# Optimization experiments

Hardware: AMD Instinct MI355X
Metric: run time of the kernel (lower is better)

## Reference

```python
import jax, jax.numpy as jnp
import numpy as np

N_TOK = 2048      # flattened batch*seq tokens
D_MODEL = 1024    # in_features
D_INT = 512       # d_intermediate
N_EXPERTS = 8     # n_routed_experts
TOP_K = 2         # n_activated_experts


def setup_inputs() -> dict:
    key = jax.random.key(0)
    k1, k2, k3, k4, k5 = jax.random.split(key, 5)
    x = jax.random.normal(k1, (N_TOK, D_MODEL), dtype=jnp.float32)
    indices = jax.random.randint(k2, (N_TOK, TOP_K), 0, N_EXPERTS, dtype=jnp.int32)
    # router combine weights (normalized over top-k like a softmax router)
    weights = jax.nn.softmax(jax.random.normal(k3, (N_TOK, TOP_K), dtype=jnp.float32), axis=-1)
    # tokens-per-expert counts, consistent with indices (as the router would supply)
    counts = jnp.bincount(indices.reshape(-1), length=N_EXPERTS).astype(jnp.int32)
    # expert weights: fc1 -> 2*d_int (gated MLP), fc2 -> d_model; kaiming-ish scale
    s1 = 1.0 / np.sqrt(D_MODEL)
    s2 = 1.0 / np.sqrt(D_INT)
    fc1_weight = jax.random.uniform(k4, (N_EXPERTS, 2 * D_INT, D_MODEL), jnp.float32, -s1, s1)
    fc2_weight = jax.random.uniform(k5, (N_EXPERTS, D_MODEL, D_INT), jnp.float32, -s2, s2)
    return {"x": x, "weights": weights, "indices": indices, "counts": counts,
            "fc1_weight": fc1_weight, "fc2_weight": fc2_weight}


def reference(x, weights, indices, counts, fc1_weight, fc2_weight):
    # Dense dispatch-free formulation: run every token through every expert's
    # gated MLP, then gather the per-slot expert output. Identical math to the
    # sort / grouped-GEMM / scatter path for the selected (token, expert) pairs.
    # h: (n_tok, n_experts, 2*d_int)
    h = jnp.einsum('td,egd->teg', x, fc1_weight)
    y, z = jnp.split(h, 2, axis=-1)
    a = y * jax.nn.silu(z)  # GatedMLP: y * activation(z)
    # expert outputs: (n_tok, n_experts, d_model)
    out = jnp.einsum('tei,edi->ted', a, fc2_weight)
    # gather the chosen expert output for each of the top-k slots: (n_tok, k, d_model)
    per_slot = jnp.take_along_axis(out, indices[:, :, None], axis=1)
    # combine: z = bmm(weights[:, None], x_by_expert).squeeze(1)
    return jnp.einsum('tk,tkd->td', weights, per_slot)
```

## Files before the change

### kernel.cpp

```cpp
#include <hip/hip_runtime.h>

typedef unsigned short u16;
typedef unsigned int u32;
using short8  = __attribute__((ext_vector_type(8))) short;
using floatx4 = __attribute__((ext_vector_type(4))) float;

#define N_TOK   2048
#define D_MODEL 1024
#define D_INT   512
#define NE      8

#define O_TOK    0
#define O_WROW   24576
#define O_XG     65536
#define O_ACT    10551296
#define O_FC1B   36765696
#define O_FC2B   53542912

static __device__ inline u16 f2bf(float f) {
    u32 u = __builtin_bit_cast(u32, f);
    u = (u + 0x7fffu + ((u >> 16) & 1u)) >> 16;
    return (u16)u;
}
static __device__ inline u32 pack2(float a, float b) {
    return (u32)f2bf(a) | ((u32)f2bf(b) << 16);
}
static __device__ inline void glds16(const u16* g, u16* l) {
    __builtin_amdgcn_global_load_lds(
        (const __attribute__((address_space(1))) void*)g,
        (__attribute__((address_space(3))) void*)l, 16, 0, 0);
}

__global__ __launch_bounds__(256) void prep_kernel(
    const float* __restrict__ x, const float* __restrict__ wts,
    const int* __restrict__ indices, const int* __restrict__ counts,
    const float* __restrict__ fc1, const float* __restrict__ fc2,
    u16* __restrict__ fc1b, u16* __restrict__ fc2b,
    u16* __restrict__ Xg, int* __restrict__ tok, float* __restrict__ wrow,
    float* __restrict__ out) {
    int b = blockIdx.x, tid = threadIdx.x;
    if (b < 6144) {
        size_t v = (size_t)b * 256 + tid;
        const float* src; u16* dst; size_t off;
        if (v < 1048576) { src = fc1; dst = fc1b; off = v * 8; }
        else             { src = fc2; dst = fc2b; off = (v - 1048576) * 8; }
        const floatx4* s4 = reinterpret_cast<const floatx4*>(src + off);
        floatx4 a = s4[0], bb = s4[1];
        uint4 o;
        o.x = pack2(a[0], a[1]); o.y = pack2(a[2], a[3]);
        o.z = pack2(bb[0], bb[1]); o.w = pack2(bb[2], bb[3]);
        *reinterpret_cast<uint4*>(dst + off) = o;
        return;
    }
    if (b < 8192) {
        int t = b - 6144;
        int off[NE];
        {
            int acc = 0;
            #pragma unroll
            for (int e = 0; e < NE; e++) { off[e] = acc; acc += ((counts[e] + 63) >> 6) << 6; }
        }
        int e0 = indices[2 * t], e1 = indices[2 * t + 1];
        __shared__ int s0, s1;
        if (tid == 0) { s0 = 0; s1 = 0; }
        __syncthreads();
        int c0 = 0, c1 = 0;
        const int4* ip = reinterpret_cast<const int4*>(indices);
        #pragma unroll
        for (int i = 0; i < 4; i++) {
            int4 vv = ip[tid * 4 + i];
            int q = tid * 16 + i * 4;
            c0 += (q + 0 < 2 * t && vv.x == e0) + (q + 1 < 2 * t && vv.y == e0)
                + (q + 2 < 2 * t && vv.z == e0) + (q + 3 < 2 * t && vv.w == e0);
            c1 += (q + 0 <= 2 * t && vv.x == e1) + (q + 1 <= 2 * t && vv.y == e1)
                + (q + 2 <= 2 * t && vv.z == e1) + (q + 3 <= 2 * t && vv.w == e1);
        }
        if (c0) atomicAdd(&s0, c0);
        if (c1) atomicAdd(&s1, c1);
        __syncthreads();
        int r0 = off[e0] + s0;
        int r1 = off[e1] + s1;
        if (tid == 0) {
            tok[r0] = t; tok[r1] = t;
            wrow[r0] = wts[2 * t]; wrow[r1] = wts[2 * t + 1];
        }
        const floatx4* src = reinterpret_cast<const floatx4*>(x + (size_t)t * D_MODEL);
        floatx4 a = src[tid];
        uint2 o;
        o.x = pack2(a[0], a[1]); o.y = pack2(a[2], a[3]);
        *reinterpret_cast<uint2*>(Xg + (size_t)r0 * D_MODEL + tid * 4) = o;
        *reinterpret_cast<uint2*>(Xg + (size_t)r1 * D_MODEL + tid * 4) = o;
        return;
    }
    {
        int z = b - 8192;
        floatx4* dst = reinterpret_cast<floatx4*>(out) + (size_t)z * 1024;
        #pragma unroll
        for (int i = 0; i < 4; i++) dst[i * 256 + tid] = (floatx4){0.f, 0.f, 0.f, 0.f};
        return;
    }
}

__global__ __launch_bounds__(256) void gemm1_kernel(
    const u16* __restrict__ Xg, const u16* __restrict__ fc1b,
    u16* __restrict__ Act, const int* __restrict__ counts) {
    __shared__ u16 As[64 * 64];
    __shared__ u16 Bs[128 * 64];
    int tid = threadIdx.x;
    int soff[NE + 1];
    {
        int acc = 0;
        #pragma unroll
        for (int e2 = 0; e2 < NE; e2++) { soff[e2] = acc; acc += ((counts[e2] + 63) >> 6) << 6; }
        soff[NE] = acc;
    }
    int row0 = blockIdx.y * 64;
    if (row0 >= soff[NE]) return;
    int e = 0;
    while (soff[e + 1] <= row0) e++;
    int bx = blockIdx.x;
    const u16* A  = Xg + (size_t)row0 * 1024;
    const u16* Be = fc1b + (size_t)e * 1024 * 1024;

    int lane = tid & 63, w = tid >> 6;
    int m0 = (w >> 1) * 32, n0 = (w & 1) * 32;
    int lr = lane & 15, kq = lane >> 4;

    const u16* gA[2]; u16* lA[2];
    #pragma unroll
    for (int j = 0; j < 2; j++) {
        int v = tid + j * 256;
        int r = v >> 3, kb = (v & 7) ^ (r & 7);
        gA[j] = A + (size_t)r * 1024 + kb * 8;
        lA[j] = As + (w * 64 + j * 256) * 8;
    }
    const u16* gB[4]; u16* lB[4];
    #pragma unroll
    for (int j = 0; j < 4; j++) {
        int v = tid + j * 256;
        int r = v >> 3, kb = (v & 7) ^ (r & 7);
        int grow = (r < 64) ? (bx * 64 + r) : (448 + bx * 64 + r);
        gB[j] = Be + (size_t)grow * 1024 + kb * 8;
        lB[j] = Bs + (w * 64 + j * 256) * 8;
    }

    floatx4 aY[2][2], aZ[2][2];
    #pragma unroll
    for (int i = 0; i < 2; i++)
        #pragma unroll
        for (int j = 0; j < 2; j++) {
            aY[i][j] = (floatx4){0.f, 0.f, 0.f, 0.f};
            aZ[i][j] = (floatx4){0.f, 0.f, 0.f, 0.f};
        }

    for (int k0 = 0; k0 < 1024; k0 += 64) {
        glds16(gA[0] + k0, lA[0]); glds16(gA[1] + k0, lA[1]);
        glds16(gB[0] + k0, lB[0]); glds16(gB[1] + k0, lB[1]);
        glds16(gB[2] + k0, lB[2]); glds16(gB[3] + k0, lB[3]);
        __syncthreads();
        #pragma unroll
        for (int ks = 0; ks < 2; ks++) {
            int sw = ((ks * 4 + kq) ^ (lr & 7)) * 8;
            short8 af[2], by[2], bz[2];
            #pragma unroll
            for (int i = 0; i < 2; i++)
                af[i] = *reinterpret_cast<const short8*>(&As[(m0 + i * 16 + lr) * 64 + sw]);
            #pragma unroll
            for (int j = 0; j < 2; j++) {
                by[j] = *reinterpret_cast<const short8*>(&Bs[(n0 + j * 16 + lr) * 64 + sw]);
                bz[j] = *reinterpret_cast<const short8*>(&Bs[(64 + n0 + j * 16 + lr) * 64 + sw]);
            }
            #pragma unroll
            for (int i = 0; i < 2; i++)
                #pragma unroll
                for (int j = 0; j < 2; j++) {
                    aY[i][j] = __builtin_amdgcn_mfma_f32_16x16x32_bf16(af[i], by[j], aY[i][j], 0, 0, 0);
                    aZ[i][j] = __builtin_amdgcn_mfma_f32_16x16x32_bf16(af[i], bz[j], aZ[i][j], 0, 0, 0);
                }
        }
        __syncthreads();
    }
    #pragma unroll
    for (int i = 0; i < 2; i++)
        #pragma unroll
        for (int j = 0; j < 2; j++) {
            floatx4 y = aY[i][j], z = aZ[i][j];
            #pragma unroll
            for (int r = 0; r < 4; r++) {
                float zz = z[r];
                float av = y[r] * (zz / (1.0f + __expf(-zz)));
                int m = m0 + i * 16 + kq * 4 + r;
                int g = bx * 64 + n0 + j * 16 + lr;
                Act[(size_t)(row0 + m) * D_INT + g] = f2bf(av);
            }
        }
}

__global__ __launch_bounds__(256) void gemm2_kernel(
    const u16* __restrict__ Act, const u16* __restrict__ fc2b,
    float* __restrict__ out, const int* __restrict__ counts,
    const int* __restrict__ tok, const float* __restrict__ wrow) {
    __shared__ u16 As[64 * 64];
    __shared__ u16 Bs[128 * 64];
    __shared__ int sTok[64];
    __shared__ float sW[64];
    int tid = threadIdx.x;
    int soff[NE + 1];
    {
        int acc = 0;
        #pragma unroll
        for (int e2 = 0; e2 < NE; e2++) { soff[e2] = acc; acc += ((counts[e2] + 63) >> 6) << 6; }
        soff[NE] = acc;
    }
    int row0 = blockIdx.y * 64;
    if (row0 >= soff[NE]) return;
    int e = 0;
    while (soff[e + 1] <= row0) e++;
    int bx = blockIdx.x;
    const u16* A  = Act + (size_t)row0 * 512;
    const u16* Be = fc2b + (size_t)e * 1024 * 512;

    int lane = tid & 63, w = tid >> 6;
    int m0 = (w >> 1) * 32, n0 = (w & 1) * 64;
    int lr = lane & 15, kq = lane >> 4;

    const u16* gA[2]; u16* lA[2];
    #pragma unroll
    for (int j = 0; j < 2; j++) {
        int v = tid + j * 256;
        int r = v >> 3, kb = (v & 7) ^ (r & 7);
        gA[j] = A + (size_t)r * 512 + kb * 8;
        lA[j] = As + (w * 64 + j * 256) * 8;
    }
    const u16* gB[4]; u16* lB[4];
    #pragma unroll
    for (int j = 0; j < 4; j++) {
        int v = tid + j * 256;
        int r = v >> 3, kb = (v & 7) ^ (r & 7);
        gB[j] = Be + (size_t)(bx * 128 + r) * 512 + kb * 8;
        lB[j] = Bs + (w * 64 + j * 256) * 8;
    }

    floatx4 acc[2][4];
    #pragma unroll
    for (int i = 0; i < 2; i++)
        #pragma unroll
        for (int j = 0; j < 4; j++) acc[i][j] = (floatx4){0.f, 0.f, 0.f, 0.f};

    for (int k0 = 0; k0 < 512; k0 += 64) {
        glds16(gA[0] + k0, lA[0]); glds16(gA[1] + k0, lA[1]);
        glds16(gB[0] + k0, lB[0]); glds16(gB[1] + k0, lB[1]);
        glds16(gB[2] + k0, lB[2]); glds16(gB[3] + k0, lB[3]);
        __syncthreads();
        #pragma unroll
        for (int ks = 0; ks < 2; ks++) {
            int sw = ((ks * 4 + kq) ^ (lr & 7)) * 8;
            short8 af[2], bf[4];
            #pragma unroll
            for (int i = 0; i < 2; i++)
                af[i] = *reinterpret_cast<const short8*>(&As[(m0 + i * 16 + lr) * 64 + sw]);
            #pragma unroll
            for (int j = 0; j < 4; j++)
                bf[j] = *reinterpret_cast<const short8*>(&Bs[(n0 + j * 16 + lr) * 64 + sw]);
            #pragma unroll
            for (int i = 0; i < 2; i++)
                #pragma unroll
                for (int j = 0; j < 4; j++)
                    acc[i][j] = __builtin_amdgcn_mfma_f32_16x16x32_bf16(af[i], bf[j], acc[i][j], 0, 0, 0);
        }
        __syncthreads();
    }
    if (tid < 64) {
        int g = row0 + tid;
        bool val = (g - soff[e]) < counts[e];
        sTok[tid] = val ? tok[g] : -1;
        sW[tid]   = val ? wrow[g] : 0.f;
    }
    __syncthreads();
    #pragma unroll
    for (int i = 0; i < 2; i++)
        #pragma unroll
        for (int r = 0; r < 4; r++) {
            int m = m0 + i * 16 + kq * 4 + r;
            int t = sTok[m];
            if (t >= 0) {
                float wgt = sW[m];
                float* dst = out + (size_t)t * D_MODEL + bx * 128;
                #pragma unroll
                for (int j = 0; j < 4; j++)
                    atomicAdd(dst + n0 + j * 16 + lr, wgt * acc[i][j][r]);
            }
        }
}

extern "C" void kernel_launch(void* const* d_in, const int* in_sizes, int n_in,
                              void* d_out, int out_size, void* d_ws, size_t ws_size,
                              hipStream_t stream) {
    const float* x       = (const float*)d_in[0];
    const float* wts     = (const float*)d_in[1];
    const int*   indices = (const int*)d_in[2];
    const int*   counts  = (const int*)d_in[3];
    const float* fc1     = (const float*)d_in[4];
    const float* fc2     = (const float*)d_in[5];
    float* out = (float*)d_out;
    char* ws = (char*)d_ws;

    int*   tok  = (int*)(ws + O_TOK);
    float* wrow = (float*)(ws + O_WROW);
    u16*   Xg   = (u16*)(ws + O_XG);
    u16*   Act  = (u16*)(ws + O_ACT);
    u16*   fc1b = (u16*)(ws + O_FC1B);
    u16*   fc2b = (u16*)(ws + O_FC2B);

    prep_kernel<<<8704, 256, 0, stream>>>(x, wts, indices, counts, fc1, fc2,
                                          fc1b, fc2b, Xg, tok, wrow, out);
    gemm1_kernel<<<dim3(8, 72), 256, 0, stream>>>(Xg, fc1b, Act, counts);
    gemm2_kernel<<<dim3(8, 72), 256, 0, stream>>>(Act, fc2b, out, counts, tok, wrow);
}
```

Measured before the change: 151.0 us.

## Double-buffer LDS tiles in both expert GEMMs to overlap loads with MFMA

Both grouped GEMM kernels now keep two LDS buffers. The next K-tile's global-to-LDS copies are issued before the MFMA work on the current tile, and an explicit vmcnt wait plus barriers stand in for the old per-iteration syncthreads. This is meant to hide global memory latency behind compute. In exchange, LDS use per block doubles, which may reduce occupancy, and correctness depends on the hand-written vmcnt counts matching the number of outstanding loads.

```diff
diff --git a/kernel.cpp b/kernel.cpp
--- a/kernel.cpp
+++ b/kernel.cpp
@@ -104,8 +104,8 @@
 __global__ __launch_bounds__(256) void gemm1_kernel(
     const u16* __restrict__ Xg, const u16* __restrict__ fc1b,
     u16* __restrict__ Act, const int* __restrict__ counts) {
-    __shared__ u16 As[64 * 64];
-    __shared__ u16 Bs[128 * 64];
+    __shared__ u16 As[2][64 * 64];
+    __shared__ u16 Bs[2][128 * 64];
     int tid = threadIdx.x;
     int soff[NE + 1];
     {
@@ -126,22 +126,22 @@
     int m0 = (w >> 1) * 32, n0 = (w & 1) * 32;
     int lr = lane & 15, kq = lane >> 4;
 
-    const u16* gA[2]; u16* lA[2];
+    const u16* gA[2]; int oA[2];
     #pragma unroll
     for (int j = 0; j < 2; j++) {
         int v = tid + j * 256;
         int r = v >> 3, kb = (v & 7) ^ (r & 7);
         gA[j] = A + (size_t)r * 1024 + kb * 8;
-        lA[j] = As + (w * 64 + j * 256) * 8;
-    }
-    const u16* gB[4]; u16* lB[4];
+        oA[j] = (w * 64 + j * 256) * 8;
+    }
+    const u16* gB[4]; int oB[4];
     #pragma unroll
     for (int j = 0; j < 4; j++) {
         int v = tid + j * 256;
         int r = v >> 3, kb = (v & 7) ^ (r & 7);
         int grow = (r < 64) ? (bx * 64 + r) : (448 + bx * 64 + r);
         gB[j] = Be + (size_t)grow * 1024 + kb * 8;
-        lB[j] = Bs + (w * 64 + j * 256) * 8;
+        oB[j] = (w * 64 + j * 256) * 8;
     }
 
     floatx4 aY[2][2], aZ[2][2];
@@ -153,22 +153,26 @@
             aZ[i][j] = (floatx4){0.f, 0.f, 0.f, 0.f};
         }
 
-    for (int k0 = 0; k0 < 1024; k0 += 64) {
-        glds16(gA[0] + k0, lA[0]); glds16(gA[1] + k0, lA[1]);
-        glds16(gB[0] + k0, lB[0]); glds16(gB[1] + k0, lB[1]);
-        glds16(gB[2] + k0, lB[2]); glds16(gB[3] + k0, lB[3]);
-        __syncthreads();
+    auto stage = [&](int bufi, int k0) {
+        glds16(gA[0] + k0, &As[bufi][oA[0]]);
+        glds16(gA[1] + k0, &As[bufi][oA[1]]);
+        glds16(gB[0] + k0, &Bs[bufi][oB[0]]);
+        glds16(gB[1] + k0, &Bs[bufi][oB[1]]);
+        glds16(gB[2] + k0, &Bs[bufi][oB[2]]);
+        glds16(gB[3] + k0, &Bs[bufi][oB[3]]);
+    };
+    auto compute = [&](int bufi) {
         #pragma unroll
         for (int ks = 0; ks < 2; ks++) {
             int sw = ((ks * 4 + kq) ^ (lr & 7)) * 8;
             short8 af[2], by[2], bz[2];
             #pragma unroll
             for (int i = 0; i < 2; i++)
-                af[i] = *reinterpret_cast<const short8*>(&As[(m0 + i * 16 + lr) * 64 + sw]);
+                af[i] = *reinterpret_cast<const short8*>(&As[bufi][(m0 + i * 16 + lr) * 64 + sw]);
             #pragma unroll
             for (int j = 0; j < 2; j++) {
-                by[j] = *reinterpret_cast<const short8*>(&Bs[(n0 + j * 16 + lr) * 64 + sw]);
-                bz[j] = *reinterpret_cast<const short8*>(&Bs[(64 + n0 + j * 16 + lr) * 64 + sw]);
+                by[j] = *reinterpret_cast<const short8*>(&Bs[bufi][(n0 + j * 16 + lr) * 64 + sw]);
+                bz[j] = *reinterpret_cast<const short8*>(&Bs[bufi][(64 + n0 + j * 16 + lr) * 64 + sw]);
             }
             #pragma unroll
             for (int i = 0; i < 2; i++)
@@ -178,8 +182,24 @@
                     aZ[i][j] = __builtin_amdgcn_mfma_f32_16x16x32_bf16(af[i], bz[j], aZ[i][j], 0, 0, 0);
                 }
         }
-        __syncthreads();
-    }
+    };
+
+    stage(0, 0);
+    int bufi = 0;
+    for (int k0 = 0; k0 < 960; k0 += 64) {
+        stage(bufi ^ 1, k0 + 64);
+        asm volatile("s_waitcnt vmcnt(6)" ::: "memory");
+        __builtin_amdgcn_s_barrier();
+        __builtin_amdgcn_sched_barrier(0);
+        compute(bufi);
+        __builtin_amdgcn_sched_barrier(0);
+        __builtin_amdgcn_s_barrier();
+        bufi ^= 1;
+    }
+    asm volatile("s_waitcnt vmcnt(0)" ::: "memory");
+    __builtin_amdgcn_s_barrier();
+    compute(bufi);
+
     #pragma unroll
     for (int i = 0; i < 2; i++)
         #pragma unroll
@@ -200,8 +220,8 @@
     const u16* __restrict__ Act, const u16* __restrict__ fc2b,
     float* __restrict__ out, const int* __restrict__ counts,
     const int* __restrict__ tok, const float* __restrict__ wrow) {
-    __shared__ u16 As[64 * 64];
-    __shared__ u16 Bs[128 * 64];
+    __shared__ u16 As[2][64 * 64];
+    __shared__ u16 Bs[2][128 * 64];
     __shared__ int sTok[64];
     __shared__ float sW[64];
     int tid = threadIdx.x;
@@ -224,58 +244,79 @@
     int m0 = (w >> 1) * 32, n0 = (w & 1) * 64;
     int lr = lane & 15, kq = lane >> 4;
 
-    const u16* gA[2]; u16* lA[2];
+    const u16* gA[2]; int oA[2];
     #pragma unroll
     for (int j = 0; j < 2; j++) {
         int v = tid + j * 256;
         int r = v >> 3, kb = (v & 7) ^ (r & 7);
         gA[j] = A + (size_t)r * 512 + kb * 8;
-        lA[j] = As + (w * 64 + j * 256) * 8;
-    }
-    const u16* gB[4]; u16* lB[4];
+        oA[j] = (w * 64 + j * 256) * 8;
+    }
+    const u16* gB[4]; int oB[4];
     #pragma unroll
     for (int j = 0; j < 4; j++) {
         int v = tid + j * 256;
         int r = v >> 3, kb = (v & 7) ^ (r & 7);
         gB[j] = Be + (size_t)(bx * 128 + r) * 512 + kb * 8;
-        lB[j] = Bs + (w * 64 + j * 256) * 8;
-    }
-
-    floatx4 acc[2][4];
-    #pragma unroll
-    for (int i = 0; i < 2; i++)
-        #pragma unroll
-        for (int j = 0; j < 4; j++) acc[i][j] = (floatx4){0.f, 0.f, 0.f, 0.f};
-
-    for (int k0 = 0; k0 < 512; k0 += 64) {
-        glds16(gA[0] + k0, lA[0]); glds16(gA[1] + k0, lA[1]);
-        glds16(gB[0] + k0, lB[0]); glds16(gB[1] + k0, lB[1]);
-        glds16(gB[2] + k0, lB[2]); glds16(gB[3] + k0, lB[3]);
-        __syncthreads();
-        #pragma unroll
-        for (int ks = 0; ks < 2; ks++) {
-            int sw = ((ks * 4 + kq) ^ (lr & 7)) * 8;
-            short8 af[2], bf[4];
-            #pragma unroll
-            for (int i = 0; i < 2; i++)
-                af[i] = *reinterpret_cast<const short8*>(&As[(m0 + i * 16 + lr) * 64 + sw]);
-            #pragma unroll
-            for (int j = 0; j < 4; j++)
-                bf[j] = *reinterpret_cast<const short8*>(&Bs[(n0 + j * 16 + lr) * 64 + sw]);
-            #pragma unroll
-            for (int i = 0; i < 2; i++)
-                #pragma unroll
-                for (int j = 0; j < 4; j++)
-                    acc[i][j] = __builtin_amdgcn_mfma_f32_16x16x32_bf16(af[i], bf[j], acc[i][j], 0, 0, 0);
-        }
-        __syncthreads();
-    }
+        oB[j] = (w * 64 + j * 256) * 8;
+    }
+
     if (tid < 64) {
         int g = row0 + tid;
         bool val = (g - soff[e]) < counts[e];
         sTok[tid] = val ? tok[g] : -1;
         sW[tid]   = val ? wrow[g] : 0.f;
     }
+
+    floatx4 acc[2][4];
+    #pragma unroll
+    for (int i = 0; i < 2; i++)
+        #pragma unroll
+        for (int j = 0; j < 4; j++) acc[i][j] = (floatx4){0.f, 0.f, 0.f, 0.f};
+
+    auto stage = [&](int bufi, int k0) {
+        glds16(gA[0] + k0, &As[bufi][oA[0]]);
+        glds16(gA[1] + k0, &As[bufi][oA[1]]);
+        glds16(gB[0] + k0, &Bs[bufi][oB[0]]);
+        glds16(gB[1] + k0, &Bs[bufi][oB[1]]);
+        glds16(gB[2] + k0, &Bs[bufi][oB[2]]);
+        glds16(gB[3] + k0, &Bs[bufi][oB[3]]);
+    };
+    auto compute = [&](int bufi) {
+        #pragma unroll
+        for (int ks = 0; ks < 2; ks++) {
+            int sw = ((ks * 4 + kq) ^ (lr & 7)) * 8;
+            short8 af[2], bfr[4];
+            #pragma unroll
+            for (int i = 0; i < 2; i++)
+                af[i] = *reinterpret_cast<const short8*>(&As[bufi][(m0 + i * 16 + lr) * 64 + sw]);
+            #pragma unroll
+            for (int j = 0; j < 4; j++)
+                bfr[j] = *reinterpret_cast<const short8*>(&Bs[bufi][(n0 + j * 16 + lr) * 64 + sw]);
+            #pragma unroll
+            for (int i = 0; i < 2; i++)
+                #pragma unroll
+                for (int j = 0; j < 4; j++)
+                    acc[i][j] = __builtin_amdgcn_mfma_f32_16x16x32_bf16(af[i], bfr[j], acc[i][j], 0, 0, 0);
+        }
+    };
+
+    stage(0, 0);
+    int bufi = 0;
+    for (int k0 = 0; k0 < 448; k0 += 64) {
+        stage(bufi ^ 1, k0 + 64);
+        asm volatile("s_waitcnt vmcnt(6)" ::: "memory");
+        __builtin_amdgcn_s_barrier();
+        __builtin_amdgcn_sched_barrier(0);
+        compute(bufi);
+        __builtin_amdgcn_sched_barrier(0);
+        __builtin_amdgcn_s_barrier();
+        bufi ^= 1;
+    }
+    asm volatile("s_waitcnt vmcnt(0)" ::: "memory");
+    __builtin_amdgcn_s_barrier();
+    compute(bufi);
+
     __syncthreads();
     #pragma unroll
     for (int i = 0; i < 2; i++)
```

Measured after the change: 152.1 us. About the same (+0.7%).

## Fuse fp32-to-bf16 weight conversion into GEMM B-tile loads with double buffering

Applied to the files above, without the earlier changes.

Removes the separate pass that converts all expert weights to bf16 in a workspace. The GEMMs now load fp32 weights directly into registers and convert them while writing the LDS tile, using double-buffered LDS so the next tile's loads overlap the current tile's MFMA work. Output zeroing moves into extra gemm1 blocks, and prep shrinks to token dispatch only. This drops a full write and re-read of the bf16 weights, but each GEMM block now reads twice the weight bytes from global memory and uses more LDS and registers.

```diff
diff --git a/kernel.cpp b/kernel.cpp
--- a/kernel.cpp
+++ b/kernel.cpp
@@ -14,8 +14,6 @@
 #define O_WROW   24576
 #define O_XG     65536
 #define O_ACT    10551296
-#define O_FC1B   36765696
-#define O_FC2B   53542912
 
 static __device__ inline u16 f2bf(float f) {
     u32 u = __builtin_bit_cast(u32, f);
@@ -34,79 +32,62 @@
 __global__ __launch_bounds__(256) void prep_kernel(
     const float* __restrict__ x, const float* __restrict__ wts,
     const int* __restrict__ indices, const int* __restrict__ counts,
-    const float* __restrict__ fc1, const float* __restrict__ fc2,
-    u16* __restrict__ fc1b, u16* __restrict__ fc2b,
-    u16* __restrict__ Xg, int* __restrict__ tok, float* __restrict__ wrow,
+    u16* __restrict__ Xg, int* __restrict__ tok, float* __restrict__ wrow) {
+    int t = blockIdx.x, tid = threadIdx.x;
+    int off[NE];
+    {
+        int acc = 0;
+        #pragma unroll
+        for (int e = 0; e < NE; e++) { off[e] = acc; acc += ((counts[e] + 63) >> 6) << 6; }
+    }
+    int e0 = indices[2 * t], e1 = indices[2 * t + 1];
+    __shared__ int s0, s1;
+    if (tid == 0) { s0 = 0; s1 = 0; }
+    __syncthreads();
+    int c0 = 0, c1 = 0;
+    const int4* ip = reinterpret_cast<const int4*>(indices);
+    #pragma unroll
+    for (int i = 0; i < 4; i++) {
+        int4 vv = ip[tid * 4 + i];
+        int q = tid * 16 + i * 4;
+        c0 += (q + 0 < 2 * t && vv.x == e0) + (q + 1 < 2 * t && vv.y == e0)
+            + (q + 2 < 2 * t && vv.z == e0) + (q + 3 < 2 * t && vv.w == e0);
+        c1 += (q + 0 <= 2 * t && vv.x == e1) + (q + 1 <= 2 * t && vv.y == e1)
+            + (q + 2 <= 2 * t && vv.z == e1) + (q + 3 <= 2 * t && vv.w == e1);
+    }
+    if (c0) atomicAdd(&s0, c0);
+    if (c1) atomicAdd(&s1, c1);
+    __syncthreads();
+    int r0 = off[e0] + s0;
+    int r1 = off[e1] + s1;
+    if (tid == 0) {
+        tok[r0] = t; tok[r1] = t;
+        wrow[r0] = wts[2 * t]; wrow[r1] = wts[2 * t + 1];
+    }
+    const floatx4* src = reinterpret_cast<const floatx4*>(x + (size_t)t * D_MODEL);
+    floatx4 a = src[tid];
+    uint2 o;
+    o.x = pack2(a[0], a[1]); o.y = pack2(a[2], a[3]);
+    *reinterpret_cast<uint2*>(Xg + (size_t)r0 * D_MODEL + tid * 4) = o;
+    *reinterpret_cast<uint2*>(Xg + (size_t)r1 * D_MODEL + tid * 4) = o;
+}
+
+__global__ __launch_bounds__(256) void gemm1_kernel(
+    const u16* __restrict__ Xg, const float* __restrict__ fc1,
+    u16* __restrict__ Act, const int* __restrict__ counts,
     float* __restrict__ out) {
-    int b = blockIdx.x, tid = threadIdx.x;
-    if (b < 6144) {
-        size_t v = (size_t)b * 256 + tid;
-        const float* src; u16* dst; size_t off;
-        if (v < 1048576) { src = fc1; dst = fc1b; off = v * 8; }
-        else             { src = fc2; dst = fc2b; off = (v - 1048576) * 8; }
-        const floatx4* s4 = reinterpret_cast<const floatx4*>(src + off);
-        floatx4 a = s4[0], bb = s4[1];
-        uint4 o;
-        o.x = pack2(a[0], a[1]); o.y = pack2(a[2], a[3]);
-        o.z = pack2(bb[0], bb[1]); o.w = pack2(bb[2], bb[3]);
-        *reinterpret_cast<uint4*>(dst + off) = o;
-        return;
-    }
-    if (b < 8192) {
-        int t = b - 6144;
-        int off[NE];
-        {
-            int acc = 0;
-            #pragma unroll
-            for (int e = 0; e < NE; e++) { off[e] = acc; acc += ((counts[e] + 63) >> 6) << 6; }
-        }
-        int e0 = indices[2 * t], e1 = indices[2 * t + 1];
-        __shared__ int s0, s1;
-        if (tid == 0) { s0 = 0; s1 = 0; }
-        __syncthreads();
-        int c0 = 0, c1 = 0;
-        const int4* ip = reinterpret_cast<const int4*>(indices);
-        #pragma unroll
-        for (int i = 0; i < 4; i++) {
-            int4 vv = ip[tid * 4 + i];
-            int q = tid * 16 + i * 4;
-            c0 += (q + 0 < 2 * t && vv.x == e0) + (q + 1 < 2 * t && vv.y == e0)
-                + (q + 2 < 2 * t && vv.z == e0) + (q + 3 < 2 * t && vv.w == e0);
-            c1 += (q + 0 <= 2 * t && vv.x == e1) + (q + 1 <= 2 * t && vv.y == e1)
-                + (q + 2 <= 2 * t && vv.z == e1) + (q + 3 <= 2 * t && vv.w == e1);
-        }
-        if (c0) atomicAdd(&s0, c0);
-        if (c1) atomicAdd(&s1, c1);
-        __syncthreads();
-        int r0 = off[e0] + s0;
-        int r1 = off[e1] + s1;
-        if (tid == 0) {
-            tok[r0] = t; tok[r1] = t;
-            wrow[r0] = wts[2 * t]; wrow[r1] = wts[2 * t + 1];
-        }
-        const floatx4* src = reinterpret_cast<const floatx4*>(x + (size_t)t * D_MODEL);
-        floatx4 a = src[tid];
-        uint2 o;
-        o.x = pack2(a[0], a[1]); o.y = pack2(a[2], a[3]);
-        *reinterpret_cast<uint2*>(Xg + (size_t)r0 * D_MODEL + tid * 4) = o;
-        *reinterpret_cast<uint2*>(Xg + (size_t)r1 * D_MODEL + tid * 4) = o;
-        return;
-    }
-    {
-        int z = b - 8192;
+    __shared__ u16 As[2][64 * 64];
+    __shared__ u16 Bs[2][128 * 64];
+    int tid = threadIdx.x;
+    int b = blockIdx.x;
+    if (b >= 576) {
+        int z = b - 576;
         floatx4* dst = reinterpret_cast<floatx4*>(out) + (size_t)z * 1024;
         #pragma unroll
         for (int i = 0; i < 4; i++) dst[i * 256 + tid] = (floatx4){0.f, 0.f, 0.f, 0.f};
         return;
     }
-}
-
-__global__ __launch_bounds__(256) void gemm1_kernel(
-    const u16* __restrict__ Xg, const u16* __restrict__ fc1b,
-    u16* __restrict__ Act, const int* __restrict__ counts) {
-    __shared__ u16 As[64 * 64];
-    __shared__ u16 Bs[128 * 64];
-    int tid = threadIdx.x;
+    int bx = b & 7, by = b >> 3;
     int soff[NE + 1];
     {
         int acc = 0;
@@ -114,34 +95,33 @@
         for (int e2 = 0; e2 < NE; e2++) { soff[e2] = acc; acc += ((counts[e2] + 63) >> 6) << 6; }
         soff[NE] = acc;
     }
-    int row0 = blockIdx.y * 64;
+    int row0 = by * 64;
     if (row0 >= soff[NE]) return;
     int e = 0;
     while (soff[e + 1] <= row0) e++;
-    int bx = blockIdx.x;
-    const u16* A  = Xg + (size_t)row0 * 1024;
-    const u16* Be = fc1b + (size_t)e * 1024 * 1024;
+    const u16*   A  = Xg + (size_t)row0 * 1024;
+    const float* Be = fc1 + (size_t)e * 1024 * 1024;
 
     int lane = tid & 63, w = tid >> 6;
     int m0 = (w >> 1) * 32, n0 = (w & 1) * 32;
     int lr = lane & 15, kq = lane >> 4;
 
-    const u16* gA[2]; u16* lA[2];
+    const u16* gA[2]; int oA[2];
     #pragma unroll
     for (int j = 0; j < 2; j++) {
         int v = tid + j * 256;
         int r = v >> 3, kb = (v & 7) ^ (r & 7);
         gA[j] = A + (size_t)r * 1024 + kb * 8;
-        lA[j] = As + (w * 64 + j * 256) * 8;
-    }
-    const u16* gB[4]; u16* lB[4];
+        oA[j] = (w * 64 + j * 256) * 8;
+    }
+    const float* gB[4]; int oBw[4];
     #pragma unroll
     for (int j = 0; j < 4; j++) {
         int v = tid + j * 256;
         int r = v >> 3, kb = (v & 7) ^ (r & 7);
         int grow = (r < 64) ? (bx * 64 + r) : (448 + bx * 64 + r);
         gB[j] = Be + (size_t)grow * 1024 + kb * 8;
-        lB[j] = Bs + (w * 64 + j * 256) * 8;
+        oBw[j] = v * 8;
     }
 
     floatx4 aY[2][2], aZ[2][2];
@@ -153,33 +133,69 @@
             aZ[i][j] = (floatx4){0.f, 0.f, 0.f, 0.f};
         }
 
-    for (int k0 = 0; k0 < 1024; k0 += 64) {
-        glds16(gA[0] + k0, lA[0]); glds16(gA[1] + k0, lA[1]);
-        glds16(gB[0] + k0, lB[0]); glds16(gB[1] + k0, lB[1]);
-        glds16(gB[2] + k0, lB[2]); glds16(gB[3] + k0, lB[3]);
-        __syncthreads();
+    auto computeT = [&](int bufi) {
         #pragma unroll
         for (int ks = 0; ks < 2; ks++) {
             int sw = ((ks * 4 + kq) ^ (lr & 7)) * 8;
-            short8 af[2], by[2], bz[2];
+            short8 af[2], byf[2], bzf[2];
             #pragma unroll
             for (int i = 0; i < 2; i++)
-                af[i] = *reinterpret_cast<const short8*>(&As[(m0 + i * 16 + lr) * 64 + sw]);
+                af[i] = *reinterpret_cast<const short8*>(&As[bufi][(m0 + i * 16 + lr) * 64 + sw]);
             #pragma unroll
             for (int j = 0; j < 2; j++) {
-                by[j] = *reinterpret_cast<const short8*>(&Bs[(n0 + j * 16 + lr) * 64 + sw]);
-                bz[j] = *reinterpret_cast<const short8*>(&Bs[(64 + n0 + j * 16 + lr) * 64 + sw]);
+                byf[j] = *reinterpret_cast<const short8*>(&Bs[bufi][(n0 + j * 16 + lr) * 64 + sw]);
+                bzf[j] = *reinterpret_cast<const short8*>(&Bs[bufi][(64 + n0 + j * 16 + lr) * 64 + sw]);
             }
             #pragma unroll
             for (int i = 0; i < 2; i++)
                 #pragma unroll
                 for (int j = 0; j < 2; j++) {
-                    aY[i][j] = __builtin_amdgcn_mfma_f32_16x16x32_bf16(af[i], by[j], aY[i][j], 0, 0, 0);
-                    aZ[i][j] = __builtin_amdgcn_mfma_f32_16x16x32_bf16(af[i], bz[j], aZ[i][j], 0, 0, 0);
+                    aY[i][j] = __builtin_amdgcn_mfma_f32_16x16x32_bf16(af[i], byf[j], aY[i][j], 0, 0, 0);
+                    aZ[i][j] = __builtin_amdgcn_mfma_f32_16x16x32_bf16(af[i], bzf[j], aZ[i][j], 0, 0, 0);
                 }
         }
+    };
+    auto stageB_write = [&](int bufi, const floatx4* lo, const floatx4* hi) {
+        #pragma unroll
+        for (int j = 0; j < 4; j++) {
+            uint4 o;
+            o.x = pack2(lo[j][0], lo[j][1]); o.y = pack2(lo[j][2], lo[j][3]);
+            o.z = pack2(hi[j][0], hi[j][1]); o.w = pack2(hi[j][2], hi[j][3]);
+            *reinterpret_cast<uint4*>(&Bs[bufi][oBw[j]]) = o;
+        }
+    };
+
+    {
+        floatx4 lo[4], hi[4];
+        #pragma unroll
+        for (int j = 0; j < 4; j++) {
+            lo[j] = *reinterpret_cast<const floatx4*>(gB[j]);
+            hi[j] = *reinterpret_cast<const floatx4*>(gB[j] + 4);
+        }
+        glds16(gA[0], &As[0][oA[0]]);
+        glds16(gA[1], &As[0][oA[1]]);
+        stageB_write(0, lo, hi);
         __syncthreads();
     }
+    int bufi = 0;
+    for (int k0 = 0; k0 < 1024; k0 += 64) {
+        int nk = k0 + 64;
+        floatx4 lo[4], hi[4];
+        if (nk < 1024) {
+            #pragma unroll
+            for (int j = 0; j < 4; j++) {
+                lo[j] = *reinterpret_cast<const floatx4*>(gB[j] + nk);
+                hi[j] = *reinterpret_cast<const floatx4*>(gB[j] + nk + 4);
+            }
+            glds16(gA[0] + nk, &As[bufi ^ 1][oA[0]]);
+            glds16(gA[1] + nk, &As[bufi ^ 1][oA[1]]);
+        }
+        computeT(bufi);
+        if (nk < 1024) stageB_write(bufi ^ 1, lo, hi);
+        __syncthreads();
+        bufi ^= 1;
+    }
+
     #pragma unroll
     for (int i = 0; i < 2; i++)
         #pragma unroll
@@ -197,14 +213,16 @@
 }
 
 __global__ __launch_bounds__(256) void gemm2_kernel(
-    const u16* __restrict__ Act, const u16* __restrict__ fc2b,
+    const u16* __restrict__ Act, const float* __restrict__ fc2,
     float* __restrict__ out, const int* __restrict__ counts,
     const int* __restrict__ tok, const float* __restrict__ wrow) {
-    __shared__ u16 As[64 * 64];
-    __shared__ u16 Bs[128 * 64];
+    __shared__ u16 As[2][64 * 64];
+    __shared__ u16 Bs[2][128 * 64];
     __shared__ int sTok[64];
     __shared__ float sW[64];
     int tid = threadIdx.x;
+    int b = blockIdx.x;
+    int bx = b & 7, by = b >> 3;
     int soff[NE + 1];
     {
         int acc = 0;
@@ -212,71 +230,106 @@
         for (int e2 = 0; e2 < NE; e2++) { soff[e2] = acc; acc += ((counts[e2] + 63) >> 6) << 6; }
         soff[NE] = acc;
     }
-    int row0 = blockIdx.y * 64;
+    int row0 = by * 64;
     if (row0 >= soff[NE]) return;
     int e = 0;
     while (soff[e + 1] <= row0) e++;
-    int bx = blockIdx.x;
-    const u16* A  = Act + (size_t)row0 * 512;
-    const u16* Be = fc2b + (size_t)e * 1024 * 512;
+    const u16*   A  = Act + (size_t)row0 * 512;
+    const float* Be = fc2 + (size_t)e * 1024 * 512;
 
     int lane = tid & 63, w = tid >> 6;
     int m0 = (w >> 1) * 32, n0 = (w & 1) * 64;
     int lr = lane & 15, kq = lane >> 4;
 
-    const u16* gA[2]; u16* lA[2];
+    const u16* gA[2]; int oA[2];
     #pragma unroll
     for (int j = 0; j < 2; j++) {
         int v = tid + j * 256;
         int r = v >> 3, kb = (v & 7) ^ (r & 7);
         gA[j] = A + (size_t)r * 512 + kb * 8;
-        lA[j] = As + (w * 64 + j * 256) * 8;
-    }
-    const u16* gB[4]; u16* lB[4];
+        oA[j] = (w * 64 + j * 256) * 8;
+    }
+    const float* gB[4]; int oBw[4];
     #pragma unroll
     for (int j = 0; j < 4; j++) {
         int v = tid + j * 256;
         int r = v >> 3, kb = (v & 7) ^ (r & 7);
         gB[j] = Be + (size_t)(bx * 128 + r) * 512 + kb * 8;
-        lB[j] = Bs + (w * 64 + j * 256) * 8;
-    }
-
-    floatx4 acc[2][4];
-    #pragma unroll
-    for (int i = 0; i < 2; i++)
-        #pragma unroll
-        for (int j = 0; j < 4; j++) acc[i][j] = (floatx4){0.f, 0.f, 0.f, 0.f};
-
-    for (int k0 = 0; k0 < 512; k0 += 64) {
-        glds16(gA[0] + k0, lA[0]); glds16(gA[1] + k0, lA[1]);
-        glds16(gB[0] + k0, lB[0]); glds16(gB[1] + k0, lB[1]);
-        glds16(gB[2] + k0, lB[2]); glds16(gB[3] + k0, lB[3]);
-        __syncthreads();
-        #pragma unroll
-        for (int ks = 0; ks < 2; ks++) {
-            int sw = ((ks * 4 + kq) ^ (lr & 7)) * 8;
-            short8 af[2], bf[4];
-            #pragma unroll
-            for (int i = 0; i < 2; i++)
-                af[i] = *reinterpret_cast<const short8*>(&As[(m0 + i * 16 + lr) * 64 + sw]);
-            #pragma unroll
-            for (int j = 0; j < 4; j++)
-                bf[j] = *reinterpret_cast<const short8*>(&Bs[(n0 + j * 16 + lr) * 64 + sw]);
-            #pragma unroll
-            for (int i = 0; i < 2; i++)
-                #pragma unroll
-                for (int j = 0; j < 4; j++)
-                    acc[i][j] = __builtin_amdgcn_mfma_f32_16x16x32_bf16(af[i], bf[j], acc[i][j], 0, 0, 0);
-        }
-        __syncthreads();
-    }
+        oBw[j] = v * 8;
+    }
+
     if (tid < 64) {
         int g = row0 + tid;
         bool val = (g - soff[e]) < counts[e];
         sTok[tid] = val ? tok[g] : -1;
         sW[tid]   = val ? wrow[g] : 0.f;
     }
-    __syncthreads();
+
+    floatx4 acc[2][4];
+    #pragma unroll
+    for (int i = 0; i < 2; i++)
+        #pragma unroll
+        for (int j = 0; j < 4; j++) acc[i][j] = (floatx4){0.f, 0.f, 0.f, 0.f};
+
+    auto computeT = [&](int bufi) {
+        #pragma unroll
+        for (int ks = 0; ks < 2; ks++) {
+            int sw = ((ks * 4 + kq) ^ (lr & 7)) * 8;
+            short8 af[2], bfr[4];
+            #pragma unroll
+            for (int i = 0; i < 2; i++)
+                af[i] = *reinterpret_cast<const short8*>(&As[bufi][(m0 + i * 16 + lr) * 64 + sw]);
+            #pragma unroll
+            for (int j = 0; j < 4; j++)
+                bfr[j] = *reinterpret_cast<const short8*>(&Bs[bufi][(n0 + j * 16 + lr) * 64 + sw]);
+            #pragma unroll
+            for (int i = 0; i < 2; i++)
+                #pragma unroll
+                for (int j = 0; j < 4; j++)
+                    acc[i][j] = __builtin_amdgcn_mfma_f32_16x16x32_bf16(af[i], bfr[j], acc[i][j], 0, 0, 0);
+        }
+    };
+    auto stageB_write = [&](int bufi, const floatx4* lo, const floatx4* hi) {
+        #pragma unroll
+        for (int j = 0; j < 4; j++) {
+            uint4 o;
+            o.x = pack2(lo[j][0], lo[j][1]); o.y = pack2(lo[j][2], lo[j][3]);
+            o.z = pack2(hi[j][0], hi[j][1]); o.w = pack2(hi[j][2], hi[j][3]);
+            *reinterpret_cast<uint4*>(&Bs[bufi][oBw[j]]) = o;
+        }
+    };
+
+    {
+        floatx4 lo[4], hi[4];
+        #pragma unroll
+        for (int j = 0; j < 4; j++) {
+            lo[j] = *reinterpret_cast<const floatx4*>(gB[j]);
+            hi[j] = *reinterpret_cast<const floatx4*>(gB[j] + 4);
+        }
+        glds16(gA[0], &As[0][oA[0]]);
+        glds16(gA[1], &As[0][oA[1]]);
+        stageB_write(0, lo, hi);
+        __syncthreads();
+    }
+    int bufi = 0;
+    for (int k0 = 0; k0 < 512; k0 += 64) {
+        int nk = k0 + 64;
+        floatx4 lo[4], hi[4];
+        if (nk < 512) {
+            #pragma unroll
+            for (int j = 0; j < 4; j++) {
+                lo[j] = *reinterpret_cast<const floatx4*>(gB[j] + nk);
+                hi[j] = *reinterpret_cast<const floatx4*>(gB[j] + nk + 4);
+            }
+            glds16(gA[0] + nk, &As[bufi ^ 1][oA[0]]);
+            glds16(gA[1] + nk, &As[bufi ^ 1][oA[1]]);
+        }
+        computeT(bufi);
+        if (nk < 512) stageB_write(bufi ^ 1, lo, hi);
+        __syncthreads();
+        bufi ^= 1;
+    }
+
     #pragma unroll
     for (int i = 0; i < 2; i++)
         #pragma unroll
@@ -309,11 +362,8 @@
     float* wrow = (float*)(ws + O_WROW);
     u16*   Xg   = (u16*)(ws + O_XG);
     u16*   Act  = (u16*)(ws + O_ACT);
-    u16*   fc1b = (u16*)(ws + O_FC1B);
-    u16*   fc2b = (u16*)(ws + O_FC2B);
-
-    prep_kernel<<<8704, 256, 0, stream>>>(x, wts, indices, counts, fc1, fc2,
-                                          fc1b, fc2b, Xg, tok, wrow, out);
-    gemm1_kernel<<<dim3(8, 72), 256, 0, stream>>>(Xg, fc1b, Act, counts);
-    gemm2_kernel<<<dim3(8, 72), 256, 0, stream>>>(Act, fc2b, out, counts, tok, wrow);
-}
+
+    prep_kernel<<<2048, 256, 0, stream>>>(x, wts, indices, counts, Xg, tok, wrow);
+    gemm1_kernel<<<1088, 256, 0, stream>>>(Xg, fc1, Act, counts, out);
+    gemm2_kernel<<<576, 256, 0, stream>>>(Act, fc2, out, counts, tok, wrow);
+}
```

New measurement: 163.7 us. 8.3% more time.
